# Optimization experiments

Hardware: AMD Instinct MI355X
Metric: run time of the kernel (lower is better)

The kernel has to match this reference:

```python
import jax, jax.numpy as jnp
import numpy as np

M, N, K, D_IN = 200, 6, 25, 784
GAMMA, EPS = 0.5, 0.5
TOTAL = M * N


def setup_inputs() -> dict:
    key = jax.random.key(0)
    ks = jax.random.split(key, 8)
    B = 16384
    def lin(kk, shape, fan_in):
        bound = 1.0 / np.sqrt(fan_in)
        return jax.random.uniform(kk, shape, jnp.float32, -bound, bound)
    return {
        "batch_x": jax.random.normal(ks[0], (B, D_IN), jnp.float32),
        "Wa": lin(ks[1], (M, D_IN), D_IN),
        "ba": lin(ks[2], (M,), D_IN),
        "Wb": lin(ks[3], (TOTAL, TOTAL), TOTAL),
        "bb": lin(ks[4], (TOTAL,), TOTAL),
        "Wd": lin(ks[5], (D_IN, M), M),
        "bd": lin(ks[6], (D_IN,), M),
    }


def _step(params, carry, x):
    Wa, ba, Wb, bb, Wd, bd = params
    x_b, phi, psi = carry
    # sigma: per-group drive broadcast over cells + full recurrent term, shape (m, n)
    z_a = (Wa @ x + ba)[:, None]                      # (m, 1)
    z_b = (Wb @ x_b + bb).reshape(M, N)               # (m, n)
    sigma = z_a + z_b
    # inhibited activity
    pi = (1.0 - phi) * (sigma - sigma.min() + 1.0)    # (m, n)
    lambda_i = pi.max(axis=1)                         # (m,)
    # top-1 cell per group (scatter of topk indices == one-hot argmax)
    M_pi = jax.nn.one_hot(jnp.argmax(pi, axis=1), N, dtype=sigma.dtype)
    # top-k groups
    _, idx = jax.lax.top_k(lambda_i, K)
    M_lambda = jnp.zeros((M,), sigma.dtype).at[idx].set(1.0)[:, None]
    y = jnp.tanh(M_pi * M_lambda * sigma)             # (m, n)
    x_a_pred = Wd @ y.max(axis=1) + bd                # (D_in,)
    # memory / inhibition updates
    psi_n = jnp.maximum(EPS * psi, y)
    phi_n = jnp.maximum(GAMMA * phi, y)
    alpha = psi_n.sum()
    alpha = jnp.where(alpha == 0.0, 1.0, alpha)
    x_b_n = (psi_n / alpha).reshape(-1)
    # original detaches the recurrent state each step
    carry_n = (jax.lax.stop_gradient(x_b_n),
               jax.lax.stop_gradient(phi_n),
               jax.lax.stop_gradient(psi_n))
    return carry_n, x_a_pred


def reference(batch_x, Wa, ba, Wb, bb, Wd, bd):
    params = (Wa, ba, Wb, bb, Wd, bd)
    carry0 = (jnp.zeros((TOTAL,), batch_x.dtype),
              jnp.zeros((M, N), batch_x.dtype),
              jnp.zeros((M, N), batch_x.dtype))
    (x_b, phi, psi), preds = jax.lax.scan(
        lambda c, x: _step(params, c, x), carry0, batch_x)
    return preds, x_b, phi, psi
```

## Files before the change

### kernel.cpp

```cpp
#include <hip/hip_runtime.h>
#include <math.h>

#define Tn   16384
#define Mg   200
#define Nc   6
#define TOT  1200
#define Kk   25
#define Din  784

__global__ void transpose_k(const float* __restrict__ src, float* __restrict__ dst,
                            int R, int C) {
    __shared__ float tile[32][33];
    int bx = blockIdx.x * 32, by = blockIdx.y * 32;
    int x = bx + threadIdx.x;
    for (int j = 0; j < 32; j += 8) {
        int y = by + threadIdx.y + j;
        if (x < C && y < R) tile[threadIdx.y + j][threadIdx.x] = src[(size_t)y * C + x];
    }
    __syncthreads();
    int x2 = by + threadIdx.x;
    for (int j = 0; j < 32; j += 8) {
        int y2 = bx + threadIdx.y + j;
        if (x2 < R && y2 < C) dst[(size_t)y2 * R + x2] = tile[threadIdx.x][threadIdx.y + j];
    }
}

__global__ void za_k(const float* __restrict__ X, const float* __restrict__ Wa,
                     const float* __restrict__ ba, float* __restrict__ Za) {
    __shared__ float xs[16][788];
    const int tid = threadIdx.x;
    const int t0  = blockIdx.x * 16;
    for (int idx = tid; idx < 16 * Din; idx += 256) {
        int tt = idx / Din, kk = idx - tt * Din;
        xs[tt][kk] = X[(size_t)(t0 + tt) * Din + kk];
    }
    __syncthreads();
    const int tq = tid & 15, gq = tid >> 4;
    const float4* xrow = reinterpret_cast<const float4*>(&xs[tq][0]);
    for (int g = gq; g < Mg; g += 16) {
        float acc = ba[g];
        const float4* wrow = reinterpret_cast<const float4*>(Wa + (size_t)g * Din);
        for (int k4 = 0; k4 < Din / 4; ++k4) {
            float4 a = xrow[k4], b = wrow[k4];
            acc = fmaf(a.x, b.x, acc); acc = fmaf(a.y, b.y, acc);
            acc = fmaf(a.z, b.z, acc); acc = fmaf(a.w, b.w, acc);
        }
        Za[(size_t)(t0 + tq) * Mg + g] = acc;
    }
}

__launch_bounds__(512, 1)
__global__ void serial_k(const float* __restrict__ Za, const float* __restrict__ WbT,
                         const float* __restrict__ bb,
                         float* __restrict__ Yval, int* __restrict__ Yidx,
                         float* __restrict__ outTail) {
    __shared__ alignas(16) unsigned long long lamk[Mg];
    __shared__ alignas(16) unsigned long long sel[26];
    __shared__ alignas(16) float red[4];
    __shared__ alignas(16) float uB[TOT];
    __shared__ int rpart[Mg];

    const int tid = threadIdx.x;
    const bool Aside = (tid < 256);
    const int g = Aside ? tid : tid - 256;
    const bool own  = (g < Mg);
    const bool ownA = Aside && own;
    const int b = Nc * g;

    float u0=0.f,u1=0.f,u2=0.f,u3=0.f,u4=0.f,u5=0.f;
    float p0=0.f,p1=0.f,p2=0.f,p3=0.f,p4=0.f,p5=0.f;
    float b0=0.f,b1=0.f,b2=0.f,b3=0.f,b4=0.f,b5=0.f;
    float alpha = 0.f, zb = 0.f;
    if (ownA) {
        b0=bb[b]; b1=bb[b+1]; b2=bb[b+2]; b3=bb[b+3]; b4=bb[b+4]; b5=bb[b+5];
        zb = Za[g];
    }
    for (int i = tid; i < TOT; i += 512) uB[i] = 0.f;
    __syncthreads();

    const float* baseW = WbT + b;

    for (int t = 0; t < Tn; ++t) {
        float zn = 0.f;
        if (ownA && t + 1 < Tn) zn = Za[(size_t)(t + 1) * Mg + g];

        unsigned long long myk = 0ull;
        float sb=0.f, pb=0.f; int bj = 0;
        float lmin = INFINITY;
        float s0=0,s1=0,s2=0,s3=0,s4=0,s5=0;
        if (ownA) {
            const float2* q = reinterpret_cast<const float2*>(&uB[b]);
            float2 q0=q[0], q1=q[1], q2=q[2];
            u0+=q0.x; u1+=q0.y; u2+=q1.x; u3+=q1.y; u4+=q2.x; u5+=q2.y;
            float inv = (alpha == 0.f) ? 1.f : (1.f / alpha);
            s0 = fmaf(u0, inv, b0 + zb); s1 = fmaf(u1, inv, b1 + zb);
            s2 = fmaf(u2, inv, b2 + zb); s3 = fmaf(u3, inv, b3 + zb);
            s4 = fmaf(u4, inv, b4 + zb); s5 = fmaf(u5, inv, b5 + zb);
            lmin = fminf(fminf(fminf(s0,s1),fminf(s2,s3)),fminf(s4,s5));
        }
        if (Aside) {
            for (int o = 32; o; o >>= 1) lmin = fminf(lmin, __shfl_down(lmin, o));
            if ((tid & 63) == 0) red[tid >> 6] = lmin;
        }
        __syncthreads();

        if (ownA) {
            float4 r4 = *reinterpret_cast<const float4*>(red);
            float m1 = 1.f - fminf(fminf(r4.x, r4.y), fminf(r4.z, r4.w));
            float best = -INFINITY;
            float sa[6] = {s0,s1,s2,s3,s4,s5};
            float pa[6] = {p0,p1,p2,p3,p4,p5};
            #pragma unroll
            for (int j = 0; j < Nc; ++j) {
                float pv = (1.f - pa[j]) * (sa[j] + m1);
                if (pv > best) { best = pv; bj = j; sb = sa[j]; pb = pa[j]; }
            }
            unsigned ub = __float_as_uint(best);
            ub ^= (unsigned)(((int)ub) >> 31) | 0x80000000u;
            myk = ((unsigned long long)ub << 32) | (unsigned long long)(0xFFFFFFFFu - (unsigned)g);
            lamk[g] = myk;
        }
        __syncthreads();

        int rr = 0; float yv = 0.f, dc = 0.f;
        if (own) {
            if (!Aside) myk = lamk[g];
            const ulonglong2* L = reinterpret_cast<const ulonglong2*>(lamk) + (Aside ? 0 : 50);
            #pragma unroll
            for (int q = 0; q < 50; ++q) {
                ulonglong2 kv = L[q];
                rr += (kv.x > myk) + (kv.y > myk);
            }
            if (ownA) { float y = tanhf(sb); yv = fmaxf(y, 0.f); dc = fmaxf(y - 0.5f * pb, 0.f); }
        }
        if (!Aside && own) rpart[g] = rr;
        __syncthreads();

        if (ownA) {
            int r = rr + rpart[g];
            float d = 0.f;
            if (r < Kk) {
                d = dc;
                sel[r] = ((unsigned long long)(unsigned)((b + bj) * TOT) << 32) |
                         (unsigned long long)__float_as_uint(d);
                Yval[(size_t)t * Kk + r] = yv;
                Yidx[(size_t)t * Kk + r] = g;
            }
            p0 = 0.5f*p0 + ((bj==0)?d:0.f); p1 = 0.5f*p1 + ((bj==1)?d:0.f);
            p2 = 0.5f*p2 + ((bj==2)?d:0.f); p3 = 0.5f*p3 + ((bj==3)?d:0.f);
            p4 = 0.5f*p4 + ((bj==4)?d:0.f); p5 = 0.5f*p5 + ((bj==5)?d:0.f);
        }
        __syncthreads();

        if (own) {
            ulonglong2 sraw[13];
            const ulonglong2* S = reinterpret_cast<const ulonglong2*>(sel);
            #pragma unroll
            for (int q = 0; q < 13; ++q) sraw[q] = S[q];
            float sd[Kk]; int so[Kk];
            #pragma unroll
            for (int k = 0; k < Kk; ++k) {
                unsigned long long v = (k & 1) ? sraw[k >> 1].y : sraw[k >> 1].x;
                sd[k] = __uint_as_float((unsigned)v);
                so[k] = (int)(v >> 32);
            }
            if (Aside) {
                float asum = 0.f;
                #pragma unroll
                for (int k = 0; k < Kk; ++k) asum += sd[k];
                alpha = 0.5f * alpha + asum;
                float2 c0[13], c1[13], c2[13];
                #pragma unroll
                for (int k = 0; k < 13; ++k) {
                    const float* cp = baseW + so[k];
                    c0[k] = *reinterpret_cast<const float2*>(cp);
                    c1[k] = *reinterpret_cast<const float2*>(cp + 2);
                    c2[k] = *reinterpret_cast<const float2*>(cp + 4);
                }
                __builtin_amdgcn_sched_barrier(0);
                float a0=0.5f*u0, a1=0.5f*u1, a2=0.5f*u2, a3=0.5f*u3, a4=0.5f*u4, a5=0.5f*u5;
                #pragma unroll
                for (int k = 0; k < 13; ++k) {
                    float dk = sd[k];
                    a0 = fmaf(dk, c0[k].x, a0); a1 = fmaf(dk, c0[k].y, a1);
                    a2 = fmaf(dk, c1[k].x, a2); a3 = fmaf(dk, c1[k].y, a3);
                    a4 = fmaf(dk, c2[k].x, a4); a5 = fmaf(dk, c2[k].y, a5);
                }
                u0=a0; u1=a1; u2=a2; u3=a3; u4=a4; u5=a5;
                zb = zn;
            } else {
                float2 c0[12], c1[12], c2[12];
                #pragma unroll
                for (int k = 0; k < 12; ++k) {
                    const float* cp = baseW + so[13 + k];
                    c0[k] = *reinterpret_cast<const float2*>(cp);
                    c1[k] = *reinterpret_cast<const float2*>(cp + 2);
                    c2[k] = *reinterpret_cast<const float2*>(cp + 4);
                }
                __builtin_amdgcn_sched_barrier(0);
                float a0=0,a1=0,a2=0,a3=0,a4=0,a5=0;
                #pragma unroll
                for (int k = 0; k < 12; ++k) {
                    float dk = sd[13 + k];
                    a0 = fmaf(dk, c0[k].x, a0); a1 = fmaf(dk, c0[k].y, a1);
                    a2 = fmaf(dk, c1[k].x, a2); a3 = fmaf(dk, c1[k].y, a3);
                    a4 = fmaf(dk, c2[k].x, a4); a5 = fmaf(dk, c2[k].y, a5);
                }
                float2* w = reinterpret_cast<float2*>(&uB[b]);
                w[0] = make_float2(a0, a1);
                w[1] = make_float2(a2, a3);
                w[2] = make_float2(a4, a5);
            }
        }
        __syncthreads();
    }

    if (ownA) {
        float inv = (alpha == 0.f) ? 1.f : (1.f / alpha);
        float pa[6] = {p0,p1,p2,p3,p4,p5};
        #pragma unroll
        for (int j = 0; j < Nc; ++j) {
            outTail[b + j]           = pa[j] * inv;
            outTail[TOT + b + j]     = pa[j];
            outTail[2 * TOT + b + j] = pa[j];
        }
    }
}

__global__ void preds_k(const float* __restrict__ Yval, const int* __restrict__ Yidx,
                        const float* __restrict__ WdT, const float* __restrict__ bd,
                        float* __restrict__ out) {
    const int t = blockIdx.x;
    __shared__ float sv[Kk];
    __shared__ int   si[Kk];
    if (threadIdx.x < Kk) {
        sv[threadIdx.x] = Yval[(size_t)t * Kk + threadIdx.x];
        si[threadIdx.x] = Yidx[(size_t)t * Kk + threadIdx.x];
    }
    __syncthreads();
    for (int d = threadIdx.x; d < Din; d += 256) {
        float acc = bd[d];
        #pragma unroll
        for (int k = 0; k < Kk; ++k)
            acc = fmaf(sv[k], WdT[(size_t)si[k] * Din + d], acc);
        out[(size_t)t * Din + d] = acc;
    }
}

extern "C" void kernel_launch(void* const* d_in, const int* in_sizes, int n_in,
                              void* d_out, int out_size, void* d_ws, size_t ws_size,
                              hipStream_t stream) {
    const float* X  = (const float*)d_in[0];
    const float* Wa = (const float*)d_in[1];
    const float* ba = (const float*)d_in[2];
    const float* Wb = (const float*)d_in[3];
    const float* bb = (const float*)d_in[4];
    const float* Wd = (const float*)d_in[5];
    const float* bd = (const float*)d_in[6];
    float* out = (float*)d_out;

    float* w    = (float*)d_ws;
    float* Za   = w;
    float* WbT  = Za  + (size_t)Tn * Mg;
    float* WdT  = WbT + (size_t)TOT * TOT;
    float* Yv   = WdT + (size_t)Mg * Din;
    int*   Yi   = (int*)(Yv + (size_t)Tn * Kk);

    dim3 tb(32, 8);
    transpose_k<<<dim3((TOT + 31) / 32, (TOT + 31) / 32), tb, 0, stream>>>(Wb, WbT, TOT, TOT);
    transpose_k<<<dim3((Mg + 31) / 32, (Din + 31) / 32), tb, 0, stream>>>(Wd, WdT, Din, Mg);
    za_k<<<Tn / 16, 256, 0, stream>>>(X, Wa, ba, Za);
    serial_k<<<1, 512, 0, stream>>>(Za, WbT, bb, Yv, Yi, out + (size_t)Tn * Din);
    preds_k<<<Tn, 256, 0, stream>>>(Yv, Yi, WdT, bd, out);
}
```

Baseline: 85.88 ms.

## Split serial recurrent step across four thread quarters instead of two halves

The single-block serial kernel grows from 512 to 1024 threads. The rank counting and the sparse Wb column gather are split four ways (4/7/7/7 selected columns), with three partial-sum buffers in shared memory that thread group 0 reduces. This shortens the per-thread dependent load and FMA chain on the latency-bound sequential path. In exchange, every barrier now synchronises more waves and group 0 does extra shared-memory reads per step.

```diff
diff --git a/kernel.cpp b/kernel.cpp
--- a/kernel.cpp
+++ b/kernel.cpp
@@ -49,7 +49,7 @@
     }
 }
 
-__launch_bounds__(512, 1)
+__launch_bounds__(1024, 4)
 __global__ void serial_k(const float* __restrict__ Za, const float* __restrict__ WbT,
                          const float* __restrict__ bb,
                          float* __restrict__ Yval, int* __restrict__ Yidx,
@@ -57,14 +57,14 @@
     __shared__ alignas(16) unsigned long long lamk[Mg];
     __shared__ alignas(16) unsigned long long sel[26];
     __shared__ alignas(16) float red[4];
-    __shared__ alignas(16) float uB[TOT];
-    __shared__ int rpart[Mg];
+    __shared__ alignas(16) float uB[3][TOT];
+    __shared__ int rpart[3][Mg];
 
     const int tid = threadIdx.x;
-    const bool Aside = (tid < 256);
-    const int g = Aside ? tid : tid - 256;
+    const int q   = tid >> 8;
+    const int g   = tid & 255;
     const bool own  = (g < Mg);
-    const bool ownA = Aside && own;
+    const bool ownA = (q == 0) && own;
     const int b = Nc * g;
 
     float u0=0.f,u1=0.f,u2=0.f,u3=0.f,u4=0.f,u5=0.f;
@@ -75,7 +75,7 @@
         b0=bb[b]; b1=bb[b+1]; b2=bb[b+2]; b3=bb[b+3]; b4=bb[b+4]; b5=bb[b+5];
         zb = Za[g];
     }
-    for (int i = tid; i < TOT; i += 512) uB[i] = 0.f;
+    for (int i = tid; i < 3 * TOT; i += 1024) (&uB[0][0])[i] = 0.f;
     __syncthreads();
 
     const float* baseW = WbT + b;
@@ -84,26 +84,32 @@
         float zn = 0.f;
         if (ownA && t + 1 < Tn) zn = Za[(size_t)(t + 1) * Mg + g];
 
+        float s0=0,s1=0,s2=0,s3=0,s4=0,s5=0;
+        if (q == 0) {
+            float lmin = INFINITY;
+            if (own) {
+                const float2* w0 = reinterpret_cast<const float2*>(&uB[0][b]);
+                const float2* w1 = reinterpret_cast<const float2*>(&uB[1][b]);
+                const float2* w2 = reinterpret_cast<const float2*>(&uB[2][b]);
+                float2 a0=w0[0], a1=w0[1], a2=w0[2];
+                float2 d0=w1[0], d1=w1[1], d2=w1[2];
+                float2 e0=w2[0], e1=w2[1], e2=w2[2];
+                u0 += a0.x + d0.x + e0.x; u1 += a0.y + d0.y + e0.y;
+                u2 += a1.x + d1.x + e1.x; u3 += a1.y + d1.y + e1.y;
+                u4 += a2.x + d2.x + e2.x; u5 += a2.y + d2.y + e2.y;
+                float inv = (alpha == 0.f) ? 1.f : (1.f / alpha);
+                s0 = fmaf(u0, inv, b0 + zb); s1 = fmaf(u1, inv, b1 + zb);
+                s2 = fmaf(u2, inv, b2 + zb); s3 = fmaf(u3, inv, b3 + zb);
+                s4 = fmaf(u4, inv, b4 + zb); s5 = fmaf(u5, inv, b5 + zb);
+                lmin = fminf(fminf(fminf(s0,s1),fminf(s2,s3)),fminf(s4,s5));
+            }
+            for (int o = 32; o; o >>= 1) lmin = fminf(lmin, __shfl_down(lmin, o));
+            if ((tid & 63) == 0) red[tid >> 6] = lmin;
+        }
+        __syncthreads();
+
         unsigned long long myk = 0ull;
         float sb=0.f, pb=0.f; int bj = 0;
-        float lmin = INFINITY;
-        float s0=0,s1=0,s2=0,s3=0,s4=0,s5=0;
-        if (ownA) {
-            const float2* q = reinterpret_cast<const float2*>(&uB[b]);
-            float2 q0=q[0], q1=q[1], q2=q[2];
-            u0+=q0.x; u1+=q0.y; u2+=q1.x; u3+=q1.y; u4+=q2.x; u5+=q2.y;
-            float inv = (alpha == 0.f) ? 1.f : (1.f / alpha);
-            s0 = fmaf(u0, inv, b0 + zb); s1 = fmaf(u1, inv, b1 + zb);
-            s2 = fmaf(u2, inv, b2 + zb); s3 = fmaf(u3, inv, b3 + zb);
-            s4 = fmaf(u4, inv, b4 + zb); s5 = fmaf(u5, inv, b5 + zb);
-            lmin = fminf(fminf(fminf(s0,s1),fminf(s2,s3)),fminf(s4,s5));
-        }
-        if (Aside) {
-            for (int o = 32; o; o >>= 1) lmin = fminf(lmin, __shfl_down(lmin, o));
-            if ((tid & 63) == 0) red[tid >> 6] = lmin;
-        }
-        __syncthreads();
-
         if (ownA) {
             float4 r4 = *reinterpret_cast<const float4*>(red);
             float m1 = 1.f - fminf(fminf(r4.x, r4.y), fminf(r4.z, r4.w));
@@ -124,20 +130,25 @@
 
         int rr = 0; float yv = 0.f, dc = 0.f;
         if (own) {
-            if (!Aside) myk = lamk[g];
-            const ulonglong2* L = reinterpret_cast<const ulonglong2*>(lamk) + (Aside ? 0 : 50);
+            if (q) myk = lamk[g];
+            const ulonglong2* L = reinterpret_cast<const ulonglong2*>(lamk) + 25 * q;
             #pragma unroll
-            for (int q = 0; q < 50; ++q) {
-                ulonglong2 kv = L[q];
+            for (int i = 0; i < 25; ++i) {
+                ulonglong2 kv = L[i];
                 rr += (kv.x > myk) + (kv.y > myk);
             }
-            if (ownA) { float y = tanhf(sb); yv = fmaxf(y, 0.f); dc = fmaxf(y - 0.5f * pb, 0.f); }
-        }
-        if (!Aside && own) rpart[g] = rr;
+            if (q == 0) {
+                float y = tanhf(sb);
+                yv = fmaxf(y, 0.f);
+                dc = fmaxf(y - 0.5f * pb, 0.f);
+            } else {
+                rpart[q - 1][g] = rr;
+            }
+        }
         __syncthreads();
 
         if (ownA) {
-            int r = rr + rpart[g];
+            int r = rr + rpart[0][g] + rpart[1][g] + rpart[2][g];
             float d = 0.f;
             if (r < Kk) {
                 d = dc;
@@ -153,25 +164,28 @@
         __syncthreads();
 
         if (own) {
-            ulonglong2 sraw[13];
             const ulonglong2* S = reinterpret_cast<const ulonglong2*>(sel);
-            #pragma unroll
-            for (int q = 0; q < 13; ++q) sraw[q] = S[q];
-            float sd[Kk]; int so[Kk];
-            #pragma unroll
-            for (int k = 0; k < Kk; ++k) {
-                unsigned long long v = (k & 1) ? sraw[k >> 1].y : sraw[k >> 1].x;
-                sd[k] = __uint_as_float((unsigned)v);
-                so[k] = (int)(v >> 32);
-            }
-            if (Aside) {
+            if (q == 0) {
+                ulonglong2 sraw[13];
+                #pragma unroll
+                for (int i = 0; i < 13; ++i) sraw[i] = S[i];
                 float asum = 0.f;
                 #pragma unroll
-                for (int k = 0; k < Kk; ++k) asum += sd[k];
+                for (int k = 0; k < Kk; ++k) {
+                    unsigned long long v = (k & 1) ? sraw[k >> 1].y : sraw[k >> 1].x;
+                    asum += __uint_as_float((unsigned)v);
+                }
                 alpha = 0.5f * alpha + asum;
-                float2 c0[13], c1[13], c2[13];
-                #pragma unroll
-                for (int k = 0; k < 13; ++k) {
+                float sd[4]; int so[4];
+                #pragma unroll
+                for (int k = 0; k < 4; ++k) {
+                    unsigned long long v = (k & 1) ? sraw[k >> 1].y : sraw[k >> 1].x;
+                    sd[k] = __uint_as_float((unsigned)v);
+                    so[k] = (int)(v >> 32);
+                }
+                float2 c0[4], c1[4], c2[4];
+                #pragma unroll
+                for (int k = 0; k < 4; ++k) {
                     const float* cp = baseW + so[k];
                     c0[k] = *reinterpret_cast<const float2*>(cp);
                     c1[k] = *reinterpret_cast<const float2*>(cp + 2);
@@ -180,7 +194,7 @@
                 __builtin_amdgcn_sched_barrier(0);
                 float a0=0.5f*u0, a1=0.5f*u1, a2=0.5f*u2, a3=0.5f*u3, a4=0.5f*u4, a5=0.5f*u5;
                 #pragma unroll
-                for (int k = 0; k < 13; ++k) {
+                for (int k = 0; k < 4; ++k) {
                     float dk = sd[k];
                     a0 = fmaf(dk, c0[k].x, a0); a1 = fmaf(dk, c0[k].y, a1);
                     a2 = fmaf(dk, c1[k].x, a2); a3 = fmaf(dk, c1[k].y, a3);
@@ -189,24 +203,38 @@
                 u0=a0; u1=a1; u2=a2; u3=a3; u4=a4; u5=a5;
                 zb = zn;
             } else {
-                float2 c0[12], c1[12], c2[12];
-                #pragma unroll
-                for (int k = 0; k < 12; ++k) {
-                    const float* cp = baseW + so[13 + k];
-                    c0[k] = *reinterpret_cast<const float2*>(cp);
-                    c1[k] = *reinterpret_cast<const float2*>(cp + 2);
-                    c2[k] = *reinterpret_cast<const float2*>(cp + 4);
+                const int k0 = 4 + 7 * (q - 1);
+                const int i0 = k0 >> 1;
+                ulonglong2 sraw[4];
+                #pragma unroll
+                for (int i = 0; i < 4; ++i) sraw[i] = S[i0 + i];
+                float sd[7]; int so[7];
+                #pragma unroll
+                for (int j = 0; j < 7; ++j) {
+                    int kk = k0 + j;
+                    unsigned long long v = (kk & 1) ? sraw[(kk >> 1) - i0].y
+                                                    : sraw[(kk >> 1) - i0].x;
+                    sd[j] = __uint_as_float((unsigned)v);
+                    so[j] = (int)(v >> 32);
+                }
+                float2 c0[7], c1[7], c2[7];
+                #pragma unroll
+                for (int j = 0; j < 7; ++j) {
+                    const float* cp = baseW + so[j];
+                    c0[j] = *reinterpret_cast<const float2*>(cp);
+                    c1[j] = *reinterpret_cast<const float2*>(cp + 2);
+                    c2[j] = *reinterpret_cast<const float2*>(cp + 4);
                 }
                 __builtin_amdgcn_sched_barrier(0);
                 float a0=0,a1=0,a2=0,a3=0,a4=0,a5=0;
                 #pragma unroll
-                for (int k = 0; k < 12; ++k) {
-                    float dk = sd[13 + k];
-                    a0 = fmaf(dk, c0[k].x, a0); a1 = fmaf(dk, c0[k].y, a1);
-                    a2 = fmaf(dk, c1[k].x, a2); a3 = fmaf(dk, c1[k].y, a3);
-                    a4 = fmaf(dk, c2[k].x, a4); a5 = fmaf(dk, c2[k].y, a5);
-                }
-                float2* w = reinterpret_cast<float2*>(&uB[b]);
+                for (int j = 0; j < 7; ++j) {
+                    float dk = sd[j];
+                    a0 = fmaf(dk, c0[j].x, a0); a1 = fmaf(dk, c0[j].y, a1);
+                    a2 = fmaf(dk, c1[j].x, a2); a3 = fmaf(dk, c1[j].y, a3);
+                    a4 = fmaf(dk, c2[j].x, a4); a5 = fmaf(dk, c2[j].y, a5);
+                }
+                float2* w = reinterpret_cast<float2*>(&uB[q - 1][b]);
                 w[0] = make_float2(a0, a1);
                 w[1] = make_float2(a2, a3);
                 w[2] = make_float2(a4, a5);
@@ -270,6 +298,6 @@
     transpose_k<<<dim3((TOT + 31) / 32, (TOT + 31) / 32), tb, 0, stream>>>(Wb, WbT, TOT, TOT);
     transpose_k<<<dim3((Mg + 31) / 32, (Din + 31) / 32), tb, 0, stream>>>(Wd, WdT, Din, Mg);
     za_k<<<Tn / 16, 256, 0, stream>>>(X, Wa, ba, Za);
-    serial_k<<<1, 512, 0, stream>>>(Za, WbT, bb, Yv, Yi, out + (size_t)Tn * Din);
+    serial_k<<<1, 1024, 0, stream>>>(Za, WbT, bb, Yv, Yi, out + (size_t)Tn * Din);
     preds_k<<<Tn, 256, 0, stream>>>(Yv, Yi, WdT, bd, out);
 }
```

Result: slower. 102.1 ms (+18.9%).
